# Kernel optimization log

Measured on AMD Instinct MI355X. Metric: run time of the kernel, lower is better.

## Reference

```python
import jax, jax.numpy as jnp
import numpy as np

ED = 1024
NH = 16
HD = ED // NH


def setup_inputs() -> dict:
    key = jax.random.key(0)
    ks = jax.random.split(key, 9)
    s = 1.0 / np.sqrt(ED)
    return {
        "x": jax.random.normal(ks[0], (2, 2048, ED), dtype=jnp.float32),
        "wq": jax.random.uniform(ks[1], (ED, ED), jnp.float32, -s, s),
        "bq": jax.random.uniform(ks[2], (ED,), jnp.float32, -s, s),
        "wk": jax.random.uniform(ks[3], (ED, ED), jnp.float32, -s, s),
        "bk": jax.random.uniform(ks[4], (ED,), jnp.float32, -s, s),
        "wv": jax.random.uniform(ks[5], (ED, ED), jnp.float32, -s, s),
        "bv": jax.random.uniform(ks[6], (ED,), jnp.float32, -s, s),
        "wo": jax.random.uniform(ks[7], (ED, ED), jnp.float32, -s, s),
        "bo": jax.random.uniform(ks[8], (ED,), jnp.float32, -s, s),
    }


def reference(x, wq, bq, wk, bk, wv, bv, wo, bo):
    B, N, _ = x.shape
    # projections; weights stored as [out, in] like nn.Linear -> x @ W.T + b
    def proj(w, b):
        y = jnp.einsum('bnd,ed->bne', x, w) + b
        return y.reshape(B, N, NH, HD).transpose(0, 2, 1, 3)  # [B, H, N, hd]
    Q, K, V = proj(wq, bq), proj(wk, bk), proj(wv, bv)
    scores = jnp.einsum('bhnd,bhmd->bhnm', Q, K) / jnp.sqrt(jnp.float32(HD))
    attn = jax.nn.softmax(scores, axis=-1)
    ctx = jnp.einsum('bhnm,bhmd->bhnd', attn, V)
    ctx = ctx.transpose(0, 2, 1, 3).reshape(B, N, ED)
    return jnp.einsum('bne,de->bnd', ctx, wo) + bo
```

## Files before the change

### kernel.cpp

```cpp
#include <hip/hip_runtime.h>
#include <hip/hip_bf16.h>

#define ED 1024
#define NH 16
#define HD 64
#define SEQ 2048

typedef float f32x4 __attribute__((ext_vector_type(4)));
typedef float f32x16 __attribute__((ext_vector_type(16)));
typedef short s16x8 __attribute__((ext_vector_type(8)));
typedef short s16x4 __attribute__((ext_vector_type(4)));
typedef __attribute__((address_space(1))) const unsigned int GBuf;
typedef __attribute__((address_space(3))) unsigned int LBuf;

#define QSC 0.18033688011112042f

union BF8 { s16x8 v; __hip_bfloat16 h[8]; };

__device__ __forceinline__ unsigned cvt_pk_bf16(float lo, float hi) {
  unsigned r;
  asm("v_cvt_pk_bf16_f32 %0, %1, %2" : "=v"(r) : "v"(lo), "v"(hi));
  return r;
}

__device__ __forceinline__ s16x8 pack_pfrag(float p0, float p1, float p2, float p3,
                                            float p4, float p5, float p6, float p7) {
  unsigned w0 = cvt_pk_bf16(p0, p1), w1 = cvt_pk_bf16(p2, p3);
  unsigned w2 = cvt_pk_bf16(p4, p5), w3 = cvt_pk_bf16(p6, p7);
  asm("v_permlane32_swap_b32 %0, %1" : "+v"(w0), "+v"(w2));
  asm("v_permlane32_swap_b32 %0, %1" : "+v"(w1), "+v"(w3));
  union { unsigned u[4]; s16x8 v; } r;
  r.u[0] = w0; r.u[1] = w1; r.u[2] = w2; r.u[3] = w3;
  return r.v;
}

__device__ inline void cvt_one(const float* __restrict__ s, __hip_bfloat16* __restrict__ d,
                               int n, int t, int stride) {
  const int n8 = n >> 3;
  for (int i = t; i < n8; i += stride) {
    const float4 u = ((const float4*)s)[2 * i];
    const float4 v = ((const float4*)s)[2 * i + 1];
    BF8 o;
    o.h[0] = __float2bfloat16(u.x); o.h[1] = __float2bfloat16(u.y);
    o.h[2] = __float2bfloat16(u.z); o.h[3] = __float2bfloat16(u.w);
    o.h[4] = __float2bfloat16(v.x); o.h[5] = __float2bfloat16(v.y);
    o.h[6] = __float2bfloat16(v.z); o.h[7] = __float2bfloat16(v.w);
    ((s16x8*)d)[i] = o.v;
  }
}

__global__ __launch_bounds__(256) void cvt5(const float* s0, const float* s1, const float* s2,
                                            const float* s3, const float* s4,
                                            __hip_bfloat16* d0, __hip_bfloat16* d1,
                                            __hip_bfloat16* d2, __hip_bfloat16* d3,
                                            __hip_bfloat16* d4,
                                            int n0, int n1, int n2, int n3, int n4) {
  const int stride = gridDim.x * blockDim.x;
  const int t = blockIdx.x * blockDim.x + threadIdx.x;
  cvt_one(s0, d0, n0, t, stride);
  cvt_one(s1, d1, n1, t, stride);
  cvt_one(s2, d2, n2, t, stride);
  cvt_one(s3, d3, n3, t, stride);
  cvt_one(s4, d4, n4, t, stride);
}

__global__ __launch_bounds__(256) void gemm_qkv(const __hip_bfloat16* __restrict__ A,
                                                const __hip_bfloat16* __restrict__ wq,
                                                const float* __restrict__ bq,
                                                const __hip_bfloat16* __restrict__ wk,
                                                const float* __restrict__ bk,
                                                const __hip_bfloat16* __restrict__ wv,
                                                const float* __restrict__ bv,
                                                __hip_bfloat16* __restrict__ Qo,
                                                __hip_bfloat16* __restrict__ Ko,
                                                __hip_bfloat16* __restrict__ Vo) {
  __shared__ __hip_bfloat16 As[2][128 * 64];
  __shared__ __hip_bfloat16 Bs[2][128 * 64];

  const int lin = (blockIdx.z * 32 + blockIdx.y) * 8 + blockIdx.x;
  const int work = (lin & 7) * 96 + (lin >> 3);
  const int z = work >> 8;
  const int rem = work & 255;
  const int m0 = (rem >> 3) * 128, n0 = (rem & 7) * 128;

  const __hip_bfloat16* W = (z == 0) ? wq : (z == 1) ? wk : wv;
  const float* bias = (z == 0) ? bq : (z == 1) ? bk : bv;

  const int tid = threadIdx.x;
  const int wave = tid >> 6, lane = tid & 63;
  const int ln15 = lane & 15, lg = lane >> 4;
  const int wr = (wave >> 1) * 64, wc = (wave & 1) * 64;

  f32x4 acc[4][4];
#pragma unroll
  for (int i = 0; i < 4; i++)
#pragma unroll
    for (int j = 0; j < 4; j++) acc[i][j] = (f32x4){0.f, 0.f, 0.f, 0.f};

  const int srow = tid >> 3;
  const int sk = (tid & 7) * 8;

  auto STAGE = [&](int t, int buf) {
    const int k0 = t * 64;
#pragma unroll
    for (int c = 0; c < 4; c++) {
      const int r = c * 32 + srow;
      __builtin_amdgcn_global_load_lds((GBuf*)(A + (size_t)(m0 + r) * ED + k0 + sk),
                                       (LBuf*)((char*)&As[buf][0] + c * 4096 + tid * 16), 16, 0, 0);
      __builtin_amdgcn_global_load_lds((GBuf*)(W + (size_t)(n0 + r) * ED + k0 + sk),
                                       (LBuf*)((char*)&Bs[buf][0] + c * 4096 + tid * 16), 16, 0, 0);
    }
  };

  const int NT = ED / 64;
  STAGE(0, 0);
  __syncthreads();
  for (int t = 0; t < NT; t++) {
    const int cur = t & 1;
    if (t + 1 < NT) STAGE(t + 1, cur ^ 1);
    __builtin_amdgcn_s_setprio(1);
#pragma unroll
    for (int kb = 0; kb < 2; kb++) {
      const int kof = kb * 32 + lg * 8;
      s16x8 a[4], b[4];
#pragma unroll
      for (int i = 0; i < 4; i++)
        a[i] = *(const s16x8*)&As[cur][(wr + i * 16 + ln15) * 64 + kof];
#pragma unroll
      for (int j = 0; j < 4; j++)
        b[j] = *(const s16x8*)&Bs[cur][(wc + j * 16 + ln15) * 64 + kof];
#pragma unroll
      for (int i = 0; i < 4; i++)
#pragma unroll
        for (int j = 0; j < 4; j++)
          acc[i][j] = __builtin_amdgcn_mfma_f32_16x16x32_bf16(a[i], b[j], acc[i][j], 0, 0, 0);
    }
    __builtin_amdgcn_s_setprio(0);
    __syncthreads();
  }

  const float scale = (z == 0) ? QSC : 1.0f;
  if (z < 2) {
    __hip_bfloat16* out = (z == 0) ? Qo : Ko;
#pragma unroll
    for (int j = 0; j < 4; j++) {
      const int e = n0 + wc + j * 16 + ln15;
      const float bvv = bias[e];
      const int h = e >> 6, hd = e & 63;
#pragma unroll
      for (int i = 0; i < 4; i++) {
#pragma unroll
        for (int r = 0; r < 4; r++) {
          const int m = m0 + wr + i * 16 + lg * 4 + r;
          const int b = m >> 11, n = m & 2047;
          out[(((size_t)(b * NH + h)) * SEQ + n) * HD + hd] =
              __float2bfloat16((acc[i][j][r] + bvv) * scale);
        }
      }
    }
  } else {
#pragma unroll
    for (int j = 0; j < 4; j++) {
      const int e = n0 + wc + j * 16 + ln15;
      const float bvv = bias[e];
      const int h = e >> 6, hd = e & 63;
#pragma unroll
      for (int i = 0; i < 4; i++) {
        const int m = m0 + wr + i * 16 + lg * 4;
        const int b = m >> 11, n = m & 2047;
        union { s16x4 v; __hip_bfloat16 hh[4]; } pk;
#pragma unroll
        for (int r = 0; r < 4; r++) pk.hh[r] = __float2bfloat16(acc[i][j][r] + bvv);
        *(s16x4*)&Vo[(((size_t)(b * NH + h)) * HD + hd) * SEQ + n] = pk.v;
      }
    }
  }
}

__global__ __launch_bounds__(256) void gemm_out(const __hip_bfloat16* __restrict__ A,
                                                const __hip_bfloat16* __restrict__ W,
                                                const float* __restrict__ bias,
                                                float* __restrict__ out) {
  __shared__ __hip_bfloat16 As[2][128 * 64];
  __shared__ __hip_bfloat16 Bs[2][128 * 64];

  const int lin = blockIdx.y * 8 + blockIdx.x;
  const int work = (lin & 7) * 32 + (lin >> 3);
  const int m0 = (work >> 3) * 128, n0 = (work & 7) * 128;

  const int tid = threadIdx.x;
  const int wave = tid >> 6, lane = tid & 63;
  const int ln15 = lane & 15, lg = lane >> 4;
  const int wr = (wave >> 1) * 64, wc = (wave & 1) * 64;

  f32x4 acc[4][4];
#pragma unroll
  for (int i = 0; i < 4; i++)
#pragma unroll
    for (int j = 0; j < 4; j++) acc[i][j] = (f32x4){0.f, 0.f, 0.f, 0.f};

  const int srow = tid >> 3;
  const int sk = (tid & 7) * 8;

  auto STAGE = [&](int t, int buf) {
    const int k0 = t * 64;
#pragma unroll
    for (int c = 0; c < 4; c++) {
      const int r = c * 32 + srow;
      __builtin_amdgcn_global_load_lds((GBuf*)(A + (size_t)(m0 + r) * ED + k0 + sk),
                                       (LBuf*)((char*)&As[buf][0] + c * 4096 + tid * 16), 16, 0, 0);
      __builtin_amdgcn_global_load_lds((GBuf*)(W + (size_t)(n0 + r) * ED + k0 + sk),
                                       (LBuf*)((char*)&Bs[buf][0] + c * 4096 + tid * 16), 16, 0, 0);
    }
  };

  const int NT = ED / 64;
  STAGE(0, 0);
  __syncthreads();
  for (int t = 0; t < NT; t++) {
    const int cur = t & 1;
    if (t + 1 < NT) STAGE(t + 1, cur ^ 1);
    __builtin_amdgcn_s_setprio(1);
#pragma unroll
    for (int kb = 0; kb < 2; kb++) {
      const int kof = kb * 32 + lg * 8;
      s16x8 a[4], b[4];
#pragma unroll
      for (int i = 0; i < 4; i++)
        a[i] = *(const s16x8*)&As[cur][(wr + i * 16 + ln15) * 64 + kof];
#pragma unroll
      for (int j = 0; j < 4; j++)
        b[j] = *(const s16x8*)&Bs[cur][(wc + j * 16 + ln15) * 64 + kof];
#pragma unroll
      for (int i = 0; i < 4; i++)
#pragma unroll
        for (int j = 0; j < 4; j++)
          acc[i][j] = __builtin_amdgcn_mfma_f32_16x16x32_bf16(a[i], b[j], acc[i][j], 0, 0, 0);
    }
    __builtin_amdgcn_s_setprio(0);
    __syncthreads();
  }

#pragma unroll
  for (int j = 0; j < 4; j++) {
    const int e = n0 + wc + j * 16 + ln15;
    const float bvv = bias[e];
#pragma unroll
    for (int i = 0; i < 4; i++)
#pragma unroll
      for (int r = 0; r < 4; r++) {
        const int m = m0 + wr + i * 16 + lg * 4 + r;
        out[(size_t)m * ED + e] = acc[i][j][r] + bvv;
      }
  }
}

__global__ __launch_bounds__(256) void attn_bf16(const __hip_bfloat16* __restrict__ Q,
                                                 const __hip_bfloat16* __restrict__ K,
                                                 const __hip_bfloat16* __restrict__ VT,
                                                 __hip_bfloat16* __restrict__ CTX) {
  __shared__ __hip_bfloat16 KsS[3][64 * 64];
  __shared__ __hip_bfloat16 VtS[3][64 * 64];

  const int tid = threadIdx.x;
  const int wave = tid >> 6, lane = tid & 63;
  const int l31 = lane & 31, hi = lane >> 5;
  const int rswz = l31 & 7;

  const int bid = blockIdx.x;
  const int work = (bid & 7) * 64 + (bid >> 3);
  const int qb = work & 15;
  const int bh = work >> 4;

  const __hip_bfloat16* Qh = Q + (size_t)bh * SEQ * HD;
  const __hip_bfloat16* Kh = K + (size_t)bh * SEQ * HD;
  const __hip_bfloat16* Vh = VT + (size_t)bh * HD * SEQ;

  const int q0 = qb * 128 + wave * 32;

  s16x8 aq[4];
#pragma unroll
  for (int kb = 0; kb < 4; kb++)
    aq[kb] = *(const s16x8*)&Qh[(size_t)(q0 + l31) * HD + kb * 16 + hi * 8];

  f32x16 acc0 = {}, acc1 = {};
  float m_ = -1e30f, l_ = 0.f;

  auto STAGE = [&](int kt_, int buf_) {
#pragma unroll
    for (int c = 0; c < 2; c++) {
      const int row = c * 32 + (tid >> 3);
      const int colb = ((tid & 7) * 16) ^ ((row & 7) << 4);
      __builtin_amdgcn_global_load_lds(
          (GBuf*)((const char*)Kh + ((size_t)(kt_ * 64 + row) * HD) * 2 + colb),
          (LBuf*)((char*)&KsS[buf_][0] + c * 4096 + tid * 16), 16, 0, 0);
      __builtin_amdgcn_global_load_lds(
          (GBuf*)((const char*)Vh + ((size_t)row * SEQ + kt_ * 64) * 2 + colb),
          (LBuf*)((char*)&VtS[buf_][0] + c * 4096 + tid * 16), 16, 0, 0);
    }
  };

  const int NT = SEQ / 64;
  STAGE(0, 0);
  STAGE(1, 1);

  for (int kt = 0; kt < NT; kt++) {
    const int cur = kt % 3;
    if (kt < NT - 1) {
      asm volatile("s_waitcnt vmcnt(4)" ::: "memory");
    } else {
      asm volatile("s_waitcnt vmcnt(0)" ::: "memory");
    }
    __builtin_amdgcn_sched_barrier(0);
    __builtin_amdgcn_s_barrier();
    if (kt + 2 < NT) STAGE(kt + 2, (kt + 2) % 3);

    f32x16 s0 = {}, s1 = {};
    __builtin_amdgcn_s_setprio(1);
#pragma unroll
    for (int kb = 0; kb < 4; kb++) {
      const int coff = ((kb * 2 + hi) ^ rswz) << 4;
      const s16x8 ak0 = *(const s16x8*)((const char*)&KsS[cur][0] + l31 * 128 + coff);
      const s16x8 ak1 = *(const s16x8*)((const char*)&KsS[cur][0] + (32 + l31) * 128 + coff);
      s0 = __builtin_amdgcn_mfma_f32_32x32x16_bf16(ak0, aq[kb], s0, 0, 0, 0);
      s1 = __builtin_amdgcn_mfma_f32_32x32x16_bf16(ak1, aq[kb], s1, 0, 0, 0);
    }
    __builtin_amdgcn_s_setprio(0);

    float t8[8];
#pragma unroll
    for (int i = 0; i < 8; i++)
      t8[i] = fmaxf(fmaxf(s0[i], s0[i + 8]), fmaxf(s1[i], s1[i + 8]));
    float tm = fmaxf(fmaxf(fmaxf(t8[0], t8[1]), fmaxf(t8[2], t8[3])),
                     fmaxf(fmaxf(t8[4], t8[5]), fmaxf(t8[6], t8[7])));
    tm = fmaxf(tm, __shfl_xor(tm, 32));

    if (!__all(tm - m_ <= 8.0f)) {
      const float mnew = fmaxf(m_, tm);
      const float fs = exp2f(m_ - mnew);
      m_ = mnew;
      l_ *= fs;
#pragma unroll
      for (int r = 0; r < 16; r++) { acc0[r] *= fs; acc1[r] *= fs; }
    }

#pragma unroll
    for (int r = 0; r < 16; r++) {
      s0[r] = exp2f(s0[r] - m_);
      s1[r] = exp2f(s1[r] - m_);
    }
    float sa[8];
#pragma unroll
    for (int i = 0; i < 8; i++) sa[i] = (s0[i] + s0[i + 8]) + (s1[i] + s1[i + 8]);
    float sum = ((sa[0] + sa[1]) + (sa[2] + sa[3])) + ((sa[4] + sa[5]) + (sa[6] + sa[7]));
    sum += __shfl_xor(sum, 32);
    l_ += sum;

    s16x8 pa[4];
    pa[0] = pack_pfrag(s0[0], s0[1], s0[2], s0[3], s0[4], s0[5], s0[6], s0[7]);
    pa[1] = pack_pfrag(s0[8], s0[9], s0[10], s0[11], s0[12], s0[13], s0[14], s0[15]);
    pa[2] = pack_pfrag(s1[0], s1[1], s1[2], s1[3], s1[4], s1[5], s1[6], s1[7]);
    pa[3] = pack_pfrag(s1[8], s1[9], s1[10], s1[11], s1[12], s1[13], s1[14], s1[15]);

    __builtin_amdgcn_s_setprio(1);
#pragma unroll
    for (int kp = 0; kp < 4; kp++) {
      const int coff = ((kp * 2 + hi) ^ rswz) << 4;
      const s16x8 av0 = *(const s16x8*)((const char*)&VtS[cur][0] + l31 * 128 + coff);
      const s16x8 av1 = *(const s16x8*)((const char*)&VtS[cur][0] + (32 + l31) * 128 + coff);
      acc0 = __builtin_amdgcn_mfma_f32_32x32x16_bf16(av0, pa[kp], acc0, 0, 0, 0);
      acc1 = __builtin_amdgcn_mfma_f32_32x32x16_bf16(av1, pa[kp], acc1, 0, 0, 0);
    }
    __builtin_amdgcn_s_setprio(0);
  }

  const float inv = 1.0f / l_;
  const int b = bh / NH, h = bh % NH;
  const int n = q0 + l31;
  __hip_bfloat16* dst = &CTX[((size_t)(b * SEQ + n)) * ED + h * HD];
#pragma unroll
  for (int g = 0; g < 4; g++) {
    union { s16x4 v; __hip_bfloat16 hh[4]; } p0, p1;
#pragma unroll
    for (int r = 0; r < 4; r++) {
      p0.hh[r] = __float2bfloat16(acc0[4 * g + r] * inv);
      p1.hh[r] = __float2bfloat16(acc1[4 * g + r] * inv);
    }
    *(s16x4*)&dst[8 * g + 4 * hi] = p0.v;
    *(s16x4*)&dst[32 + 8 * g + 4 * hi] = p1.v;
  }
}

extern "C" void kernel_launch(void* const* d_in, const int* in_sizes, int n_in,
                              void* d_out, int out_size, void* d_ws, size_t ws_size,
                              hipStream_t stream) {
  const float* x = (const float*)d_in[0];
  const float* wq = (const float*)d_in[1];
  const float* bq = (const float*)d_in[2];
  const float* wk = (const float*)d_in[3];
  const float* bk = (const float*)d_in[4];
  const float* wv = (const float*)d_in[5];
  const float* bv = (const float*)d_in[6];
  const float* wo = (const float*)d_in[7];
  const float* bo = (const float*)d_in[8];
  float* out = (float*)d_out;

  const int BN = in_sizes[0] / ED;

  char* w = (char*)d_ws;
  __hip_bfloat16* xbf = (__hip_bfloat16*)(w);
  __hip_bfloat16* wqb = (__hip_bfloat16*)(w + (8 << 20));
  __hip_bfloat16* wkb = (__hip_bfloat16*)(w + (10 << 20));
  __hip_bfloat16* wvb = (__hip_bfloat16*)(w + (12 << 20));
  __hip_bfloat16* wob = (__hip_bfloat16*)(w + (14 << 20));
  __hip_bfloat16* Qb = (__hip_bfloat16*)(w + (16 << 20));
  __hip_bfloat16* Kb = (__hip_bfloat16*)(w + (24 << 20));
  __hip_bfloat16* VTb = (__hip_bfloat16*)(w + (32 << 20));
  __hip_bfloat16* CTXb = (__hip_bfloat16*)(w + (40 << 20));

  cvt5<<<1024, 256, 0, stream>>>(x, wq, wk, wv, wo, xbf, wqb, wkb, wvb, wob,
                                 BN * ED, ED * ED, ED * ED, ED * ED, ED * ED);

  const dim3 blk(256);
  gemm_qkv<<<dim3(ED / 128, BN / 128, 3), blk, 0, stream>>>(
      xbf, wqb, bq, wkb, bk, wvb, bv, Qb, Kb, VTb);

  attn_bf16<<<dim3(512), blk, 0, stream>>>(Qb, Kb, VTb, CTXb);

  gemm_out<<<dim3(ED / 128, BN / 128), blk, 0, stream>>>(CTXb, wob, bo, out);
}
```

Measured before the change: 237.7 us.

## Use 256x256 GEMM tiles with 512 threads and split-KV attention within block

Both projection GEMMs move from 128x128 tiles with 256 threads to 256x256 tiles with 512 threads and a K-step of 32, which doubles per-wave accumulators and gives fewer, larger blocks. The attention kernel now runs 8 waves: two groups each process alternating KV tiles for the same queries, then merge partial softmax state through LDS. The aim is more compute per global load and more waves per block, at the cost of higher register pressure, far fewer GEMM blocks than CUs (192 and 64), and a merge step at the end of attention.

After: 237.4 us. Within noise of the previous version (-0.2%).

```diff
diff --git a/kernel.cpp b/kernel.cpp
--- a/kernel.cpp
+++ b/kernel.cpp
@@ -64,7 +64,7 @@
   cvt_one(s4, d4, n4, t, stride);
 }
 
-__global__ __launch_bounds__(256) void gemm_qkv(const __hip_bfloat16* __restrict__ A,
+__global__ __launch_bounds__(512) void gemm_qkv(const __hip_bfloat16* __restrict__ A,
                                                 const __hip_bfloat16* __restrict__ wq,
                                                 const float* __restrict__ bq,
                                                 const __hip_bfloat16* __restrict__ wk,
@@ -74,14 +74,14 @@
                                                 __hip_bfloat16* __restrict__ Qo,
                                                 __hip_bfloat16* __restrict__ Ko,
                                                 __hip_bfloat16* __restrict__ Vo) {
-  __shared__ __hip_bfloat16 As[2][128 * 64];
-  __shared__ __hip_bfloat16 Bs[2][128 * 64];
-
-  const int lin = (blockIdx.z * 32 + blockIdx.y) * 8 + blockIdx.x;
-  const int work = (lin & 7) * 96 + (lin >> 3);
-  const int z = work >> 8;
-  const int rem = work & 255;
-  const int m0 = (rem >> 3) * 128, n0 = (rem & 7) * 128;
+  __shared__ __hip_bfloat16 As[2][256 * 32];
+  __shared__ __hip_bfloat16 Bs[2][256 * 32];
+
+  const int lin = blockIdx.x;
+  const int work = (lin & 7) * 24 + (lin >> 3);
+  const int z = work >> 6;
+  const int rem = work & 63;
+  const int m0 = (rem >> 2) * 256, n0 = (rem & 3) * 256;
 
   const __hip_bfloat16* W = (z == 0) ? wq : (z == 1) ? wk : wv;
   const float* bias = (z == 0) ? bq : (z == 1) ? bk : bv;
@@ -89,52 +89,48 @@
   const int tid = threadIdx.x;
   const int wave = tid >> 6, lane = tid & 63;
   const int ln15 = lane & 15, lg = lane >> 4;
-  const int wr = (wave >> 1) * 64, wc = (wave & 1) * 64;
-
-  f32x4 acc[4][4];
-#pragma unroll
-  for (int i = 0; i < 4; i++)
+  const int wr = (wave >> 2) * 128, wc = (wave & 3) * 64;
+
+  f32x4 acc[8][4];
+#pragma unroll
+  for (int i = 0; i < 8; i++)
 #pragma unroll
     for (int j = 0; j < 4; j++) acc[i][j] = (f32x4){0.f, 0.f, 0.f, 0.f};
 
-  const int srow = tid >> 3;
-  const int sk = (tid & 7) * 8;
+  const int srow = tid >> 2;
+  const int sk = (tid & 3) * 8;
 
   auto STAGE = [&](int t, int buf) {
-    const int k0 = t * 64;
-#pragma unroll
-    for (int c = 0; c < 4; c++) {
-      const int r = c * 32 + srow;
+    const int k0 = t * 32;
+#pragma unroll
+    for (int c = 0; c < 2; c++) {
+      const int r = c * 128 + srow;
       __builtin_amdgcn_global_load_lds((GBuf*)(A + (size_t)(m0 + r) * ED + k0 + sk),
-                                       (LBuf*)((char*)&As[buf][0] + c * 4096 + tid * 16), 16, 0, 0);
+                                       (LBuf*)((char*)&As[buf][0] + c * 8192 + tid * 16), 16, 0, 0);
       __builtin_amdgcn_global_load_lds((GBuf*)(W + (size_t)(n0 + r) * ED + k0 + sk),
-                                       (LBuf*)((char*)&Bs[buf][0] + c * 4096 + tid * 16), 16, 0, 0);
+                                       (LBuf*)((char*)&Bs[buf][0] + c * 8192 + tid * 16), 16, 0, 0);
     }
   };
 
-  const int NT = ED / 64;
+  const int NT = ED / 32;
   STAGE(0, 0);
   __syncthreads();
   for (int t = 0; t < NT; t++) {
     const int cur = t & 1;
     if (t + 1 < NT) STAGE(t + 1, cur ^ 1);
     __builtin_amdgcn_s_setprio(1);
-#pragma unroll
-    for (int kb = 0; kb < 2; kb++) {
-      const int kof = kb * 32 + lg * 8;
-      s16x8 a[4], b[4];
-#pragma unroll
-      for (int i = 0; i < 4; i++)
-        a[i] = *(const s16x8*)&As[cur][(wr + i * 16 + ln15) * 64 + kof];
+    s16x8 a[8], b[4];
+#pragma unroll
+    for (int i = 0; i < 8; i++)
+      a[i] = *(const s16x8*)&As[cur][(wr + i * 16 + ln15) * 32 + lg * 8];
+#pragma unroll
+    for (int j = 0; j < 4; j++)
+      b[j] = *(const s16x8*)&Bs[cur][(wc + j * 16 + ln15) * 32 + lg * 8];
+#pragma unroll
+    for (int i = 0; i < 8; i++)
 #pragma unroll
       for (int j = 0; j < 4; j++)
-        b[j] = *(const s16x8*)&Bs[cur][(wc + j * 16 + ln15) * 64 + kof];
-#pragma unroll
-      for (int i = 0; i < 4; i++)
-#pragma unroll
-        for (int j = 0; j < 4; j++)
-          acc[i][j] = __builtin_amdgcn_mfma_f32_16x16x32_bf16(a[i], b[j], acc[i][j], 0, 0, 0);
-    }
+        acc[i][j] = __builtin_amdgcn_mfma_f32_16x16x32_bf16(a[i], b[j], acc[i][j], 0, 0, 0);
     __builtin_amdgcn_s_setprio(0);
     __syncthreads();
   }
@@ -148,7 +144,7 @@
       const float bvv = bias[e];
       const int h = e >> 6, hd = e & 63;
 #pragma unroll
-      for (int i = 0; i < 4; i++) {
+      for (int i = 0; i < 8; i++) {
 #pragma unroll
         for (int r = 0; r < 4; r++) {
           const int m = m0 + wr + i * 16 + lg * 4 + r;
@@ -165,7 +161,7 @@
       const float bvv = bias[e];
       const int h = e >> 6, hd = e & 63;
 #pragma unroll
-      for (int i = 0; i < 4; i++) {
+      for (int i = 0; i < 8; i++) {
         const int m = m0 + wr + i * 16 + lg * 4;
         const int b = m >> 11, n = m & 2047;
         union { s16x4 v; __hip_bfloat16 hh[4]; } pk;
@@ -177,66 +173,62 @@
   }
 }
 
-__global__ __launch_bounds__(256) void gemm_out(const __hip_bfloat16* __restrict__ A,
+__global__ __launch_bounds__(512) void gemm_out(const __hip_bfloat16* __restrict__ A,
                                                 const __hip_bfloat16* __restrict__ W,
                                                 const float* __restrict__ bias,
                                                 float* __restrict__ out) {
-  __shared__ __hip_bfloat16 As[2][128 * 64];
-  __shared__ __hip_bfloat16 Bs[2][128 * 64];
-
-  const int lin = blockIdx.y * 8 + blockIdx.x;
-  const int work = (lin & 7) * 32 + (lin >> 3);
-  const int m0 = (work >> 3) * 128, n0 = (work & 7) * 128;
+  __shared__ __hip_bfloat16 As[2][256 * 32];
+  __shared__ __hip_bfloat16 Bs[2][256 * 32];
+
+  const int lin = blockIdx.x;
+  const int work = (lin & 7) * 8 + (lin >> 3);
+  const int m0 = (work >> 2) * 256, n0 = (work & 3) * 256;
 
   const int tid = threadIdx.x;
   const int wave = tid >> 6, lane = tid & 63;
   const int ln15 = lane & 15, lg = lane >> 4;
-  const int wr = (wave >> 1) * 64, wc = (wave & 1) * 64;
-
-  f32x4 acc[4][4];
-#pragma unroll
-  for (int i = 0; i < 4; i++)
+  const int wr = (wave >> 2) * 128, wc = (wave & 3) * 64;
+
+  f32x4 acc[8][4];
+#pragma unroll
+  for (int i = 0; i < 8; i++)
 #pragma unroll
     for (int j = 0; j < 4; j++) acc[i][j] = (f32x4){0.f, 0.f, 0.f, 0.f};
 
-  const int srow = tid >> 3;
-  const int sk = (tid & 7) * 8;
+  const int srow = tid >> 2;
+  const int sk = (tid & 3) * 8;
 
   auto STAGE = [&](int t, int buf) {
-    const int k0 = t * 64;
-#pragma unroll
-    for (int c = 0; c < 4; c++) {
-      const int r = c * 32 + srow;
+    const int k0 = t * 32;
+#pragma unroll
+    for (int c = 0; c < 2; c++) {
+      const int r = c * 128 + srow;
       __builtin_amdgcn_global_load_lds((GBuf*)(A + (size_t)(m0 + r) * ED + k0 + sk),
-                                       (LBuf*)((char*)&As[buf][0] + c * 4096 + tid * 16), 16, 0, 0);
+                                       (LBuf*)((char*)&As[buf][0] + c * 8192 + tid * 16), 16, 0, 0);
       __builtin_amdgcn_global_load_lds((GBuf*)(W + (size_t)(n0 + r) * ED + k0 + sk),
-                                       (LBuf*)((char*)&Bs[buf][0] + c * 4096 + tid * 16), 16, 0, 0);
+                                       (LBuf*)((char*)&Bs[buf][0] + c * 8192 + tid * 16), 16, 0, 0);
     }
   };
 
-  const int NT = ED / 64;
+  const int NT = ED / 32;
   STAGE(0, 0);
   __syncthreads();
   for (int t = 0; t < NT; t++) {
     const int cur = t & 1;
     if (t + 1 < NT) STAGE(t + 1, cur ^ 1);
     __builtin_amdgcn_s_setprio(1);
-#pragma unroll
-    for (int kb = 0; kb < 2; kb++) {
-      const int kof = kb * 32 + lg * 8;
-      s16x8 a[4], b[4];
-#pragma unroll
-      for (int i = 0; i < 4; i++)
-        a[i] = *(const s16x8*)&As[cur][(wr + i * 16 + ln15) * 64 + kof];
+    s16x8 a[8], b[4];
+#pragma unroll
+    for (int i = 0; i < 8; i++)
+      a[i] = *(const s16x8*)&As[cur][(wr + i * 16 + ln15) * 32 + lg * 8];
+#pragma unroll
+    for (int j = 0; j < 4; j++)
+      b[j] = *(const s16x8*)&Bs[cur][(wc + j * 16 + ln15) * 32 + lg * 8];
+#pragma unroll
+    for (int i = 0; i < 8; i++)
 #pragma unroll
       for (int j = 0; j < 4; j++)
-        b[j] = *(const s16x8*)&Bs[cur][(wc + j * 16 + ln15) * 64 + kof];
-#pragma unroll
-      for (int i = 0; i < 4; i++)
-#pragma unroll
-        for (int j = 0; j < 4; j++)
-          acc[i][j] = __builtin_amdgcn_mfma_f32_16x16x32_bf16(a[i], b[j], acc[i][j], 0, 0, 0);
-    }
+        acc[i][j] = __builtin_amdgcn_mfma_f32_16x16x32_bf16(a[i], b[j], acc[i][j], 0, 0, 0);
     __builtin_amdgcn_s_setprio(0);
     __syncthreads();
   }
@@ -246,7 +238,7 @@
     const int e = n0 + wc + j * 16 + ln15;
     const float bvv = bias[e];
 #pragma unroll
-    for (int i = 0; i < 4; i++)
+    for (int i = 0; i < 8; i++)
 #pragma unroll
       for (int r = 0; r < 4; r++) {
         const int m = m0 + wr + i * 16 + lg * 4 + r;
@@ -255,17 +247,20 @@
   }
 }
 
-__global__ __launch_bounds__(256) void attn_bf16(const __hip_bfloat16* __restrict__ Q,
-                                                 const __hip_bfloat16* __restrict__ K,
-                                                 const __hip_bfloat16* __restrict__ VT,
-                                                 __hip_bfloat16* __restrict__ CTX) {
-  __shared__ __hip_bfloat16 KsS[3][64 * 64];
-  __shared__ __hip_bfloat16 VtS[3][64 * 64];
+__global__ __launch_bounds__(512, 4) void attn_bf16(const __hip_bfloat16* __restrict__ Q,
+                                                    const __hip_bfloat16* __restrict__ K,
+                                                    const __hip_bfloat16* __restrict__ VT,
+                                                    __hip_bfloat16* __restrict__ CTX) {
+  __shared__ char ldsraw[65536];
+  float* mgacc = (float*)ldsraw;
+  float* mgml = (float*)(ldsraw + 4 * 32 * 66 * 4);
 
   const int tid = threadIdx.x;
   const int wave = tid >> 6, lane = tid & 63;
   const int l31 = lane & 31, hi = lane >> 5;
   const int rswz = l31 & 7;
+  const int par = wave >> 2;
+  const int wq = wave & 3;
 
   const int bid = blockIdx.x;
   const int work = (bid & 7) * 64 + (bid >> 3);
@@ -276,7 +271,7 @@
   const __hip_bfloat16* Kh = K + (size_t)bh * SEQ * HD;
   const __hip_bfloat16* Vh = VT + (size_t)bh * HD * SEQ;
 
-  const int q0 = qb * 128 + wave * 32;
+  const int q0 = qb * 128 + wq * 32;
 
   s16x8 aq[4];
 #pragma unroll
@@ -286,42 +281,40 @@
   f32x16 acc0 = {}, acc1 = {};
   float m_ = -1e30f, l_ = 0.f;
 
-  auto STAGE = [&](int kt_, int buf_) {
+  const int lt = tid & 255;
+  auto STAGE = [&](int tile, int buf) {
 #pragma unroll
     for (int c = 0; c < 2; c++) {
-      const int row = c * 32 + (tid >> 3);
-      const int colb = ((tid & 7) * 16) ^ ((row & 7) << 4);
+      const int row = c * 32 + (lt >> 3);
+      const int colb = ((lt & 7) * 16) ^ ((row & 7) << 4);
+      char* kbase = ldsraw + ((par * 2 + buf) * 2 + 0) * 8192;
+      char* vbase = ldsraw + ((par * 2 + buf) * 2 + 1) * 8192;
       __builtin_amdgcn_global_load_lds(
-          (GBuf*)((const char*)Kh + ((size_t)(kt_ * 64 + row) * HD) * 2 + colb),
-          (LBuf*)((char*)&KsS[buf_][0] + c * 4096 + tid * 16), 16, 0, 0);
+          (GBuf*)((const char*)Kh + ((size_t)(tile * 64 + row) * HD) * 2 + colb),
+          (LBuf*)(kbase + c * 4096 + lt * 16), 16, 0, 0);
       __builtin_amdgcn_global_load_lds(
-          (GBuf*)((const char*)Vh + ((size_t)row * SEQ + kt_ * 64) * 2 + colb),
-          (LBuf*)((char*)&VtS[buf_][0] + c * 4096 + tid * 16), 16, 0, 0);
+          (GBuf*)((const char*)Vh + ((size_t)row * SEQ + tile * 64) * 2 + colb),
+          (LBuf*)(vbase + c * 4096 + lt * 16), 16, 0, 0);
     }
   };
 
-  const int NT = SEQ / 64;
-  STAGE(0, 0);
-  STAGE(1, 1);
-
-  for (int kt = 0; kt < NT; kt++) {
-    const int cur = kt % 3;
-    if (kt < NT - 1) {
-      asm volatile("s_waitcnt vmcnt(4)" ::: "memory");
-    } else {
-      asm volatile("s_waitcnt vmcnt(0)" ::: "memory");
-    }
-    __builtin_amdgcn_sched_barrier(0);
-    __builtin_amdgcn_s_barrier();
-    if (kt + 2 < NT) STAGE(kt + 2, (kt + 2) % 3);
+  const int NI = SEQ / 128;
+  STAGE(par, 0);
+  for (int i = 0; i < NI; i++) {
+    const int cur = i & 1;
+    __syncthreads();
+    if (i + 1 < NI) STAGE(2 * (i + 1) + par, cur ^ 1);
+
+    const char* Ksb = ldsraw + ((par * 2 + cur) * 2 + 0) * 8192;
+    const char* Vtb = ldsraw + ((par * 2 + cur) * 2 + 1) * 8192;
 
     f32x16 s0 = {}, s1 = {};
     __builtin_amdgcn_s_setprio(1);
 #pragma unroll
     for (int kb = 0; kb < 4; kb++) {
       const int coff = ((kb * 2 + hi) ^ rswz) << 4;
-      const s16x8 ak0 = *(const s16x8*)((const char*)&KsS[cur][0] + l31 * 128 + coff);
-      const s16x8 ak1 = *(const s16x8*)((const char*)&KsS[cur][0] + (32 + l31) * 128 + coff);
+      const s16x8 ak0 = *(const s16x8*)(Ksb + l31 * 128 + coff);
+      const s16x8 ak1 = *(const s16x8*)(Ksb + (32 + l31) * 128 + coff);
       s0 = __builtin_amdgcn_mfma_f32_32x32x16_bf16(ak0, aq[kb], s0, 0, 0, 0);
       s1 = __builtin_amdgcn_mfma_f32_32x32x16_bf16(ak1, aq[kb], s1, 0, 0, 0);
     }
@@ -329,8 +322,8 @@
 
     float t8[8];
 #pragma unroll
-    for (int i = 0; i < 8; i++)
-      t8[i] = fmaxf(fmaxf(s0[i], s0[i + 8]), fmaxf(s1[i], s1[i + 8]));
+    for (int i2 = 0; i2 < 8; i2++)
+      t8[i2] = fmaxf(fmaxf(s0[i2], s0[i2 + 8]), fmaxf(s1[i2], s1[i2 + 8]));
     float tm = fmaxf(fmaxf(fmaxf(t8[0], t8[1]), fmaxf(t8[2], t8[3])),
                      fmaxf(fmaxf(t8[4], t8[5]), fmaxf(t8[6], t8[7])));
     tm = fmaxf(tm, __shfl_xor(tm, 32));
@@ -351,7 +344,7 @@
     }
     float sa[8];
 #pragma unroll
-    for (int i = 0; i < 8; i++) sa[i] = (s0[i] + s0[i + 8]) + (s1[i] + s1[i + 8]);
+    for (int i2 = 0; i2 < 8; i2++) sa[i2] = (s0[i2] + s0[i2 + 8]) + (s1[i2] + s1[i2 + 8]);
     float sum = ((sa[0] + sa[1]) + (sa[2] + sa[3])) + ((sa[4] + sa[5]) + (sa[6] + sa[7]));
     sum += __shfl_xor(sum, 32);
     l_ += sum;
@@ -366,28 +359,55 @@
 #pragma unroll
     for (int kp = 0; kp < 4; kp++) {
       const int coff = ((kp * 2 + hi) ^ rswz) << 4;
-      const s16x8 av0 = *(const s16x8*)((const char*)&VtS[cur][0] + l31 * 128 + coff);
-      const s16x8 av1 = *(const s16x8*)((const char*)&VtS[cur][0] + (32 + l31) * 128 + coff);
+      const s16x8 av0 = *(const s16x8*)(Vtb + l31 * 128 + coff);
+      const s16x8 av1 = *(const s16x8*)(Vtb + (32 + l31) * 128 + coff);
       acc0 = __builtin_amdgcn_mfma_f32_32x32x16_bf16(av0, pa[kp], acc0, 0, 0, 0);
       acc1 = __builtin_amdgcn_mfma_f32_32x32x16_bf16(av1, pa[kp], acc1, 0, 0, 0);
     }
     __builtin_amdgcn_s_setprio(0);
   }
 
-  const float inv = 1.0f / l_;
-  const int b = bh / NH, h = bh % NH;
-  const int n = q0 + l31;
-  __hip_bfloat16* dst = &CTX[((size_t)(b * SEQ + n)) * ED + h * HD];
-#pragma unroll
-  for (int g = 0; g < 4; g++) {
-    union { s16x4 v; __hip_bfloat16 hh[4]; } p0, p1;
-#pragma unroll
-    for (int r = 0; r < 4; r++) {
-      p0.hh[r] = __float2bfloat16(acc0[4 * g + r] * inv);
-      p1.hh[r] = __float2bfloat16(acc1[4 * g + r] * inv);
-    }
-    *(s16x4*)&dst[8 * g + 4 * hi] = p0.v;
-    *(s16x4*)&dst[32 + 8 * g + 4 * hi] = p1.v;
+  __syncthreads();
+  if (wave >= 4) {
+    const int w = wave - 4;
+    float* ap = &mgacc[(w * 32 + l31) * 66];
+#pragma unroll
+    for (int g = 0; g < 4; g++)
+#pragma unroll
+      for (int r = 0; r < 4; r++) {
+        ap[8 * g + 4 * hi + r] = acc0[4 * g + r];
+        ap[32 + 8 * g + 4 * hi + r] = acc1[4 * g + r];
+      }
+    if (hi == 0) {
+      mgml[(w * 2 + 0) * 32 + l31] = m_;
+      mgml[(w * 2 + 1) * 32 + l31] = l_;
+    }
+  }
+  __syncthreads();
+  if (wave < 4) {
+    const float m1 = mgml[(wave * 2 + 0) * 32 + l31];
+    const float l1 = mgml[(wave * 2 + 1) * 32 + l31];
+    const float mm = fmaxf(m_, m1);
+    const float f0 = exp2f(m_ - mm), f1 = exp2f(m1 - mm);
+    const float inv = 1.0f / (l_ * f0 + l1 * f1);
+    const float* ap = &mgacc[(wave * 32 + l31) * 66];
+
+    const int b = bh / NH, h = bh % NH;
+    const int n = q0 + l31;
+    __hip_bfloat16* dst = &CTX[((size_t)(b * SEQ + n)) * ED + h * HD];
+#pragma unroll
+    for (int g = 0; g < 4; g++) {
+      union { s16x4 v; __hip_bfloat16 hh[4]; } p0, p1;
+#pragma unroll
+      for (int r = 0; r < 4; r++) {
+        const float o0 = (acc0[4 * g + r] * f0 + ap[8 * g + 4 * hi + r] * f1) * inv;
+        const float o1 = (acc1[4 * g + r] * f0 + ap[32 + 8 * g + 4 * hi + r] * f1) * inv;
+        p0.hh[r] = __float2bfloat16(o0);
+        p1.hh[r] = __float2bfloat16(o1);
+      }
+      *(s16x4*)&dst[8 * g + 4 * hi] = p0.v;
+      *(s16x4*)&dst[32 + 8 * g + 4 * hi] = p1.v;
+    }
   }
 }
 
@@ -421,11 +441,10 @@
   cvt5<<<1024, 256, 0, stream>>>(x, wq, wk, wv, wo, xbf, wqb, wkb, wvb, wob,
                                  BN * ED, ED * ED, ED * ED, ED * ED, ED * ED);
 
-  const dim3 blk(256);
-  gemm_qkv<<<dim3(ED / 128, BN / 128, 3), blk, 0, stream>>>(
+  gemm_qkv<<<dim3(192), dim3(512), 0, stream>>>(
       xbf, wqb, bq, wkb, bk, wvb, bv, Qb, Kb, VTb);
 
-  attn_bf16<<<dim3(512), blk, 0, stream>>>(Qb, Kb, VTb, CTXb);
-
-  gemm_out<<<dim3(ED / 128, BN / 128), blk, 0, stream>>>(CTXb, wob, bo, out);
-}
+  attn_bf16<<<dim3(512), dim3(512), 0, stream>>>(Qb, Kb, VTb, CTXb);
+
+  gemm_out<<<dim3(64), dim3(512), 0, stream>>>(CTXb, wob, bo, out);
+}
```
